# Kernel tuning notes

Measured on AMD Instinct MI355X. Metric: run time of the kernel, lower is better.

## Reference

```python
import jax, jax.numpy as jnp
import numpy as np
import math


def _unfold(x, k, s, p):
    # torch nn.Unfold: output [B, C*k*k, L] with channel-major (c, kh, kw) ordering,
    # which matches lax.conv_general_dilated_patches channel ordering.
    patches = jax.lax.conv_general_dilated_patches(
        x, (k, k), (s, s), [(p, p), (p, p)],
        dimension_numbers=('NCHW', 'OIHW', 'NCHW'))
    B, C, H, W = patches.shape
    return patches.reshape(B, C, H * W).transpose(0, 2, 1)  # [B, L, C*k*k]


def _ln(x, g, b):
    mu = x.mean(-1, keepdims=True)
    var = ((x - mu) ** 2).mean(-1, keepdims=True)
    return (x - mu) * jax.lax.rsqrt(var + 1e-5) * g + b


def _prm_exp(x, w):
    # FAVOR+ positive random-feature map: exp(w@x - |x|^2/2)/sqrt(m)
    m = w.shape[0]
    xd = (x * x).sum(-1, keepdims=True) * 0.5          # [B,T,1]
    wtx = jnp.einsum('btd,md->btm', x, w)              # [B,T,m]
    return jnp.exp(wtx - xd) / jnp.sqrt(jnp.float32(m))


def _performer(x, p):
    (kqv_w, kqv_b, proj_w, proj_b, ln1_g, ln1_b, ln2_g, ln2_b,
     m1_w, m1_b, m2_w, m2_b, rf_w) = p
    emb = proj_w.shape[0]
    xn = _ln(x, ln1_g, ln1_b)
    kqv = xn @ kqv_w + kqv_b
    k, q, v = kqv[..., :emb], kqv[..., emb:2 * emb], kqv[..., 2 * emb:]
    kp, qp = _prm_exp(k, rf_w), _prm_exp(q, rf_w)      # [B,T,m]
    D = jnp.einsum('btm,bm->bt', qp, kp.sum(1))[..., None]   # [B,T,1]
    kptv = jnp.einsum('btn,btm->bnm', v, kp)                 # [B,emb,m]
    y = jnp.einsum('btm,bnm->btn', qp, kptv) / (D + 1e-8)    # [B,T,emb]
    y = v + (y @ proj_w + proj_b)                            # dropout = identity (eval)
    h = jax.nn.gelu(_ln(y, ln2_g, ln2_b) @ m1_w + m1_b, approximate=False) @ m2_w + m2_b
    return y + h


def setup_inputs() -> dict:
    key = jax.random.key(0)
    B, emb, m = 64, 64, 32

    def lin(k, din, dout):
        return jax.random.normal(k, (din, dout), jnp.float32) / np.sqrt(din).astype(np.float32)

    def orth(seed, dim_in):
        a = np.random.default_rng(seed).standard_normal((dim_in, m))
        q, _ = np.linalg.qr(a)  # columns orthonormal
        return jnp.asarray((q[:, :m].T * np.sqrt(m)).astype(np.float32))  # [m, emb]

    inp = {"x": jax.random.normal(jax.random.fold_in(key, 0), (B, 3, 224, 224), jnp.float32)}
    for i, d in ((1, 147), (2, 576)):
        pre = f"p{i}_"
        k1, k2, k3, k4 = jax.random.split(jax.random.fold_in(key, i), 4)
        inp[pre + "kqv_w"] = lin(k1, d, 3 * emb); inp[pre + "kqv_b"] = jnp.zeros(3 * emb, jnp.float32)
        inp[pre + "proj_w"] = lin(k2, emb, emb);  inp[pre + "proj_b"] = jnp.zeros(emb, jnp.float32)
        inp[pre + "ln1_g"] = jnp.ones(d, jnp.float32);   inp[pre + "ln1_b"] = jnp.zeros(d, jnp.float32)
        inp[pre + "ln2_g"] = jnp.ones(emb, jnp.float32); inp[pre + "ln2_b"] = jnp.zeros(emb, jnp.float32)
        inp[pre + "m1_w"] = lin(k3, emb, emb); inp[pre + "m1_b"] = jnp.zeros(emb, jnp.float32)
        inp[pre + "m2_w"] = lin(k4, emb, emb); inp[pre + "m2_b"] = jnp.zeros(emb, jnp.float32)
        inp[pre + "rf"] = orth(100 + i, emb)
    inp["proj_w"] = lin(jax.random.fold_in(key, 99), 576, 768)
    inp["proj_b"] = jnp.zeros(768, jnp.float32)
    return inp


def reference(x,
              p1_kqv_w, p1_kqv_b, p1_proj_w, p1_proj_b, p1_ln1_g, p1_ln1_b,
              p1_ln2_g, p1_ln2_b, p1_m1_w, p1_m1_b, p1_m2_w, p1_m2_b, p1_rf,
              p2_kqv_w, p2_kqv_b, p2_proj_w, p2_proj_b, p2_ln1_g, p2_ln1_b,
              p2_ln2_g, p2_ln2_b, p2_m1_w, p2_m1_b, p2_m2_w, p2_m2_b, p2_rf,
              proj_w, proj_b):
    p1 = (p1_kqv_w, p1_kqv_b, p1_proj_w, p1_proj_b, p1_ln1_g, p1_ln1_b,
          p1_ln2_g, p1_ln2_b, p1_m1_w, p1_m1_b, p1_m2_w, p1_m2_b, p1_rf)
    p2 = (p2_kqv_w, p2_kqv_b, p2_proj_w, p2_proj_b, p2_ln1_g, p2_ln1_b,
          p2_ln2_g, p2_ln2_b, p2_m1_w, p2_m1_b, p2_m2_w, p2_m2_b, p2_rf)
    h = _unfold(x, 7, 4, 2)                 # [B, 3136, 147]
    h = _performer(h, p1)                   # [B, 3136, 64]
    B, T, C = h.shape
    s = int(math.isqrt(T))
    h = h.transpose(0, 2, 1).reshape(B, C, s, s)   # [B,64,56,56]
    h = _unfold(h, 3, 2, 1)                 # [B, 784, 576]
    h = _performer(h, p2)                   # [B, 784, 64]
    B, T, C = h.shape
    s = int(math.isqrt(T))
    h = h.transpose(0, 2, 1).reshape(B, C, s, s)   # [B,64,28,28]
    h = _unfold(h, 3, 2, 1)                 # [B, 196, 576]
    return h @ proj_w + proj_b              # [B, 196, 768]
```

## Files before the change

kernel.cpp:

```cpp
#include <hip/hip_runtime.h>
#include <hip/hip_bf16.h>

#define NB 64
#define T1 3136
#define T2 784
#define T3 196
#define D1 147
#define D2 576

#define KP1 160
#define KS1 168
#define KS2 584
#define KQ2 72

typedef __attribute__((ext_vector_type(8))) short bf16x8;
typedef __attribute__((ext_vector_type(4))) float f32x4;

__device__ __forceinline__ unsigned short f2bf(float v) {
    unsigned int u = __float_as_uint(v);
    return (unsigned short)((u + 0x7FFFu + ((u >> 16) & 1u)) >> 16);
}

__device__ __forceinline__ float waveReduceSum(float v) {
#pragma unroll
    for (int off = 32; off > 0; off >>= 1) v += __shfl_down(v, off, 64);
    return __shfl(v, 0, 64);
}

__global__ __launch_bounds__(192) void prep_sums(
    const float* __restrict__ w, const float* __restrict__ g,
    const float* __restrict__ bb, const float* __restrict__ kqvb,
    float* __restrict__ s2, float* __restrict__ s3, int D)
{
    const int col = threadIdx.x;
    const int d0 = blockIdx.x * 16;
    const int d1 = (d0 + 16 < D) ? d0 + 16 : D;
    float a2 = 0.f, a3 = 0.f;
    for (int d = d0; d < d1; ++d) {
        const float wv = w[d * 192 + col];
        a2 += wv * g[d];
        a3 += wv * bb[d];
    }
    if (blockIdx.x == 0) a3 += kqvb[col];
    atomicAdd(&s2[col], a2);
    atomicAdd(&s3[col], a3);
}

__global__ __launch_bounds__(256) void prep_wt(
    const float* __restrict__ w, const float* __restrict__ g,
    unsigned short* __restrict__ hi, unsigned short* __restrict__ lo,
    int D, int K, int N)
{
    const int i = blockIdx.x * 256 + threadIdx.x;
    if (i >= N * K) return;
    const int n = i / K, k = i % K;
    const float v = (k < D) ? w[k * N + n] * (g ? g[k] : 1.f) : 0.f;
    const unsigned short h = f2bf(v);
    const float hf = __uint_as_float((unsigned int)h << 16);
    const size_t pidx = (size_t)((n >> 4) * (K >> 5) + (k >> 5)) * 512
                      + (size_t)((((k >> 3) & 3) * 16 + (n & 15)) * 8 + (k & 7));
    hi[pidx] = h;
    lo[pidx] = f2bf(v - hf);
}

__global__ __launch_bounds__(256) void prep_rf(
    const float* __restrict__ rf,
    unsigned short* __restrict__ hi, unsigned short* __restrict__ lo)
{
    const int i = blockIdx.x * 256 + threadIdx.x;
    if (i >= 2048) return;
    const int n = i >> 6, k = i & 63;
    const float v = rf[i];
    const unsigned short h = f2bf(v);
    const float hf = __uint_as_float((unsigned int)h << 16);
    const int pidx = ((n >> 4) * 2 + (k >> 5)) * 512
                   + ((((k >> 3) & 3) * 16 + (n & 15)) * 8 + (k & 7));
    hi[pidx] = h;
    lo[pidx] = f2bf(v - hf);
}

__global__ __launch_bounds__(256) void front1(
    const float* __restrict__ x,
    const unsigned short* __restrict__ wt_hi,
    const unsigned short* __restrict__ wt_lo,
    const float* __restrict__ s2v, const float* __restrict__ s3v,
    const unsigned short* __restrict__ rf_hi,
    const unsigned short* __restrict__ rf_lo,
    float* __restrict__ kp, float* __restrict__ qp,
    float* __restrict__ v_out)
{
    const int tok0 = blockIdx.x * 32;
    const int b = tok0 / T1;
    const int tbase = tok0 % T1;
    const int tid = threadIdx.x;
    const int wv = tid >> 6, l = tid & 63;
    const int l15 = l & 15, lg = l >> 4;

    __shared__ __align__(16) unsigned short Abuf[2 * 32 * KS1];
    __shared__ float ps_sum[256], ps_sq[256];
    __shared__ float mu_s[32], rs_s[32], xd_s[64];

    unsigned short* A_hi = Abuf;
    unsigned short* A_lo = Abuf + 32 * KS1;
    unsigned short* kqh = Abuf;
    unsigned short* kql = Abuf + 64 * KQ2;

    { const int m = tid >> 3, j = tid & 7;
      const int t = tbase + m;
      const int py = t / 56, px = t % 56;
      const int iy0 = py * 4 - 2, ix0 = px * 4 - 2;
      float sm = 0.f, sq = 0.f;
      for (int d = j; d < KS1; d += 8) {
          float val = 0.f;
          if (d < D1) {
              const int cc = d / 49, r = d % 49, ki = r / 7, kj = r % 7;
              const int iy = iy0 + ki, ix = ix0 + kj;
              if (iy >= 0 && iy < 224 && ix >= 0 && ix < 224)
                  val = x[((b * 3 + cc) * 224 + iy) * 224 + ix];
          }
          sm += val; sq += val * val;
          const unsigned short h = f2bf(val);
          A_hi[m * KS1 + d] = h;
          A_lo[m * KS1 + d] = f2bf(val - __uint_as_float((unsigned int)h << 16));
      }
      ps_sum[tid] = sm; ps_sq[tid] = sq; }
    __syncthreads();
    if (tid < 32) {
        float s = 0.f, s2 = 0.f;
#pragma unroll
        for (int j2 = 0; j2 < 8; ++j2) { s += ps_sum[tid*8+j2]; s2 += ps_sq[tid*8+j2]; }
        const float mu = s * (1.f / D1);
        mu_s[tid] = mu; rs_s[tid] = rsqrtf(s2 * (1.f / D1) - mu * mu + 1e-5f);
    }

    f32x4 acc[2][3];
    { const f32x4 z = {0.f, 0.f, 0.f, 0.f};
#pragma unroll
      for (int mt = 0; mt < 2; ++mt)
#pragma unroll
        for (int nt = 0; nt < 3; ++nt) acc[mt][nt] = z; }

    for (int ks = 0; ks < 5; ++ks) {
        const int ko = ks * 32 + 8 * lg;
        const bf16x8 ah0 = *(const bf16x8*)&A_hi[l15 * KS1 + ko];
        const bf16x8 ah1 = *(const bf16x8*)&A_hi[(16 + l15) * KS1 + ko];
        const bf16x8 al0 = *(const bf16x8*)&A_lo[l15 * KS1 + ko];
        const bf16x8 al1 = *(const bf16x8*)&A_lo[(16 + l15) * KS1 + ko];
#pragma unroll
        for (int nt = 0; nt < 3; ++nt) {
            const size_t wo = ((size_t)((3 * wv + nt) * 5 + ks) << 9) + (size_t)(l << 3);
            const bf16x8 bh = *(const bf16x8*)&wt_hi[wo];
            const bf16x8 bl = *(const bf16x8*)&wt_lo[wo];
            acc[0][nt] = __builtin_amdgcn_mfma_f32_16x16x32_bf16(ah0, bh, acc[0][nt], 0, 0, 0);
            acc[1][nt] = __builtin_amdgcn_mfma_f32_16x16x32_bf16(ah1, bh, acc[1][nt], 0, 0, 0);
            acc[0][nt] = __builtin_amdgcn_mfma_f32_16x16x32_bf16(al0, bh, acc[0][nt], 0, 0, 0);
            acc[1][nt] = __builtin_amdgcn_mfma_f32_16x16x32_bf16(al1, bh, acc[1][nt], 0, 0, 0);
            acc[0][nt] = __builtin_amdgcn_mfma_f32_16x16x32_bf16(ah0, bl, acc[0][nt], 0, 0, 0);
            acc[1][nt] = __builtin_amdgcn_mfma_f32_16x16x32_bf16(ah1, bl, acc[1][nt], 0, 0, 0);
        }
    }
    __syncthreads();

    float xk[2][4], xq[2][4];
#pragma unroll
    for (int mt = 0; mt < 2; ++mt)
#pragma unroll
        for (int r = 0; r < 4; ++r) { xk[mt][r] = 0.f; xq[mt][r] = 0.f; }

#pragma unroll
    for (int nt = 0; nt < 3; ++nt) {
        const int col = 48 * wv + 16 * nt + l15;
        const int third = col >> 6, cc = col & 63;
        const float s2c = s2v[col], s3c = s3v[col];
#pragma unroll
        for (int mt = 0; mt < 2; ++mt) {
#pragma unroll
            for (int r = 0; r < 4; ++r) {
                const int token = mt * 16 + 4 * lg + r;
                const float o = rs_s[token] * (acc[mt][nt][r] - mu_s[token] * s2c) + s3c;
                if (third == 2) {
                    v_out[(size_t)(tok0 + token) * 64 + cc] = o;
                } else {
                    const int row = third * 32 + token;
                    const unsigned short h = f2bf(o);
                    kqh[row * KQ2 + cc] = h;
                    kql[row * KQ2 + cc] = f2bf(o - __uint_as_float((unsigned int)h << 16));
                    if (third == 0) xk[mt][r] += o * o; else xq[mt][r] += o * o;
                }
            }
        }
    }
#pragma unroll
    for (int mt = 0; mt < 2; ++mt) {
#pragma unroll
        for (int r = 0; r < 4; ++r) {
            float a = xk[mt][r], q2 = xq[mt][r];
#pragma unroll
            for (int off = 1; off < 16; off <<= 1) {
                a  += __shfl_xor(a,  off, 64);
                q2 += __shfl_xor(q2, off, 64);
            }
            if (l15 == 0) {
                const int token = mt * 16 + 4 * lg + r;
                ps_sum[wv * 64 + token]      = a;
                ps_sum[wv * 64 + 32 + token] = q2;
            }
        }
    }
    __syncthreads();
    if (tid < 64)
        xd_s[tid] = 0.5f * (ps_sum[tid] + ps_sum[64+tid] + ps_sum[128+tid] + ps_sum[192+tid]);
    __syncthreads();

    f32x4 pacc[2];
    { const f32x4 z = {0.f, 0.f, 0.f, 0.f}; pacc[0] = z; pacc[1] = z; }
#pragma unroll
    for (int ks = 0; ks < 2; ++ks) {
        const int ko = ks * 32 + 8 * lg;
        const bf16x8 ah = *(const bf16x8*)&kqh[(16 * wv + l15) * KQ2 + ko];
        const bf16x8 al = *(const bf16x8*)&kql[(16 * wv + l15) * KQ2 + ko];
#pragma unroll
        for (int nt = 0; nt < 2; ++nt) {
            const int wo = (nt * 2 + ks) * 512 + l * 8;
            const bf16x8 bh = *(const bf16x8*)&rf_hi[wo];
            const bf16x8 bl = *(const bf16x8*)&rf_lo[wo];
            pacc[nt] = __builtin_amdgcn_mfma_f32_16x16x32_bf16(ah, bh, pacc[nt], 0, 0, 0);
            pacc[nt] = __builtin_amdgcn_mfma_f32_16x16x32_bf16(al, bh, pacc[nt], 0, 0, 0);
            pacc[nt] = __builtin_amdgcn_mfma_f32_16x16x32_bf16(ah, bl, pacc[nt], 0, 0, 0);
        }
    }
#pragma unroll
    for (int nt = 0; nt < 2; ++nt) {
#pragma unroll
        for (int r = 0; r < 4; ++r) {
            const int row = 16 * wv + 4 * lg + r;
            const int half = row >> 5, token = row & 31;
            const float p = expf(pacc[nt][r] - xd_s[row]) * 0.1767766952966369f;
            (half ? qp : kp)[(size_t)(tok0 + token) * 32 + nt * 16 + l15] = p;
        }
    }
}

__global__ __launch_bounds__(256) void front2(
    const float* __restrict__ src,
    const unsigned short* __restrict__ wt_hi,
    const unsigned short* __restrict__ wt_lo,
    const float* __restrict__ s2v, const float* __restrict__ s3v,
    const unsigned short* __restrict__ rf_hi,
    const unsigned short* __restrict__ rf_lo,
    float* __restrict__ kp, float* __restrict__ qp,
    float* __restrict__ v_out)
{
    const int tok0 = blockIdx.x * 16;
    const int b = tok0 / T2;
    const int tbase = tok0 % T2;
    const int tid = threadIdx.x;
    const int wv = tid >> 6, l = tid & 63;
    const int l15 = l & 15, lg = l >> 4;

    __shared__ __align__(16) unsigned short Abuf[2 * 16 * KS2];
    __shared__ float ps_sum[256], ps_sq[256];
    __shared__ float mu_s[16], rs_s[16], xd_s[32];

    unsigned short* A_hi = Abuf;
    unsigned short* A_lo = Abuf + 16 * KS2;
    unsigned short* kqh = Abuf;
    unsigned short* kql = Abuf + 32 * KQ2;

    { const int g16 = tid >> 4, ch = tid & 15;
      const int tmine = tbase + g16;
      const int py = tmine / 28, px = tmine % 28;
      const int iy0 = py * 2 - 1, ix0 = px * 2 - 1;
      const float* srcb = src + (size_t)b * T1 * 64 + ch;
      unsigned short* Ah = &A_hi[g16 * KS2];
      unsigned short* Al = &A_lo[g16 * KS2];
      float sm = 0.f, sq = 0.f;
#pragma unroll
      for (int r = 0; r < 9; ++r) {
          const int iy = iy0 + r / 3, ix = ix0 + r % 3;
          const bool ok = (iy >= 0 && iy < 56 && ix >= 0 && ix < 56);
          const float* sp = srcb + (size_t)(iy * 56 + ix) * 64;
#pragma unroll
          for (int c = 0; c < 4; ++c) {
              const float val = ok ? sp[c * 16] : 0.f;
              sm += val; sq += val * val;
              const int d = (c * 16 + ch) * 9 + r;
              const unsigned short h = f2bf(val);
              Ah[d] = h;
              Al[d] = f2bf(val - __uint_as_float((unsigned int)h << 16));
          }
      }
      ps_sum[tid] = sm; ps_sq[tid] = sq; }
    __syncthreads();
    if (tid < 16) {
        float s = 0.f, s2 = 0.f;
#pragma unroll
        for (int j = 0; j < 16; ++j) { s += ps_sum[tid*16+j]; s2 += ps_sq[tid*16+j]; }
        const float mu = s * (1.f / D2);
        mu_s[tid] = mu; rs_s[tid] = rsqrtf(s2 * (1.f / D2) - mu * mu + 1e-5f);
    }

    f32x4 acc[3];
    { const f32x4 z = {0.f, 0.f, 0.f, 0.f};
#pragma unroll
      for (int nt = 0; nt < 3; ++nt) acc[nt] = z; }

    for (int ks = 0; ks < 18; ++ks) {
        const int ko = ks * 32 + 8 * lg;
        const bf16x8 ah = *(const bf16x8*)&A_hi[l15 * KS2 + ko];
        const bf16x8 al = *(const bf16x8*)&A_lo[l15 * KS2 + ko];
#pragma unroll
        for (int nt = 0; nt < 3; ++nt) {
            const size_t wo = ((size_t)((3 * wv + nt) * 18 + ks) << 9) + (size_t)(l << 3);
            const bf16x8 bh = *(const bf16x8*)&wt_hi[wo];
            const bf16x8 bl = *(const bf16x8*)&wt_lo[wo];
            acc[nt] = __builtin_amdgcn_mfma_f32_16x16x32_bf16(ah, bh, acc[nt], 0, 0, 0);
            acc[nt] = __builtin_amdgcn_mfma_f32_16x16x32_bf16(al, bh, acc[nt], 0, 0, 0);
            acc[nt] = __builtin_amdgcn_mfma_f32_16x16x32_bf16(ah, bl, acc[nt], 0, 0, 0);
        }
    }
    __syncthreads();

    float xk[4], xq[4];
#pragma unroll
    for (int r = 0; r < 4; ++r) { xk[r] = 0.f; xq[r] = 0.f; }

#pragma unroll
    for (int nt = 0; nt < 3; ++nt) {
        const int col = 48 * wv + 16 * nt + l15;
        const int third = col >> 6, cc = col & 63;
        const float s2c = s2v[col], s3c = s3v[col];
#pragma unroll
        for (int r = 0; r < 4; ++r) {
            const int token = 4 * lg + r;
            const float o = rs_s[token] * (acc[nt][r] - mu_s[token] * s2c) + s3c;
            if (third == 2) {
                v_out[(size_t)(tok0 + token) * 64 + cc] = o;
            } else {
                const int row = third * 16 + token;
                const unsigned short h = f2bf(o);
                kqh[row * KQ2 + cc] = h;
                kql[row * KQ2 + cc] = f2bf(o - __uint_as_float((unsigned int)h << 16));
                if (third == 0) xk[r] += o * o; else xq[r] += o * o;
            }
        }
    }
#pragma unroll
    for (int r = 0; r < 4; ++r) {
        float a = xk[r], q2 = xq[r];
#pragma unroll
        for (int off = 1; off < 16; off <<= 1) {
            a  += __shfl_xor(a,  off, 64);
            q2 += __shfl_xor(q2, off, 64);
        }
        if (l15 == 0) {
            const int token = 4 * lg + r;
            ps_sum[wv * 64 + token]      = a;
            ps_sum[wv * 64 + 16 + token] = q2;
        }
    }
    __syncthreads();
    if (tid < 32)
        xd_s[tid] = 0.5f * (ps_sum[tid] + ps_sum[64+tid] + ps_sum[128+tid] + ps_sum[192+tid]);
    __syncthreads();

    const int mt = wv >> 1, ntp = wv & 1;
    f32x4 pacc;
    { const f32x4 z = {0.f, 0.f, 0.f, 0.f}; pacc = z; }
#pragma unroll
    for (int ks = 0; ks < 2; ++ks) {
        const int ko = ks * 32 + 8 * lg;
        const bf16x8 ah = *(const bf16x8*)&kqh[(16 * mt + l15) * KQ2 + ko];
        const bf16x8 al = *(const bf16x8*)&kql[(16 * mt + l15) * KQ2 + ko];
        const int wo = (ntp * 2 + ks) * 512 + l * 8;
        const bf16x8 bh = *(const bf16x8*)&rf_hi[wo];
        const bf16x8 bl = *(const bf16x8*)&rf_lo[wo];
        pacc = __builtin_amdgcn_mfma_f32_16x16x32_bf16(ah, bh, pacc, 0, 0, 0);
        pacc = __builtin_amdgcn_mfma_f32_16x16x32_bf16(al, bh, pacc, 0, 0, 0);
        pacc = __builtin_amdgcn_mfma_f32_16x16x32_bf16(ah, bl, pacc, 0, 0, 0);
    }
#pragma unroll
    for (int r = 0; r < 4; ++r) {
        const int row = 16 * mt + 4 * lg + r;
        const int half = row >> 4, token = row & 15;
        const float p = expf(pacc[r] - xd_s[row]) * 0.1767766952966369f;
        (half ? qp : kp)[(size_t)(tok0 + token) * 32 + ntp * 16 + l15] = p;
    }
}

template <int T, int S>
__global__ __launch_bounds__(256) void reduce_kv(
    const float* __restrict__ kp, const float* __restrict__ v,
    float* __restrict__ ksum, float* __restrict__ kptv)
{
    const int b = blockIdx.x / S, s = blockIdx.x % S;
    const int chunk = T / S;
    const int tid = threadIdx.x;
    __shared__ float kp_s[8][32];
    __shared__ float v_s[8][64];
    float acc[8] = {0.f, 0.f, 0.f, 0.f, 0.f, 0.f, 0.f, 0.f};
    float ks = 0.f;
    const int n = tid >> 2;
    const int mb = (tid & 3) * 8;
    const float* kpb = kp + (size_t)b * T * 32;
    const float* vb  = v  + (size_t)b * T * 64;

    for (int t0 = s * chunk; t0 < (s + 1) * chunk; t0 += 8) {
        kp_s[tid >> 5][tid & 31] = kpb[(t0 + (tid >> 5)) * 32 + (tid & 31)];
        {
            const int i0 = tid * 2, i1 = tid * 2 + 1;
            v_s[i0 >> 6][i0 & 63] = vb[(t0 + (i0 >> 6)) * 64 + (i0 & 63)];
            v_s[i1 >> 6][i1 & 63] = vb[(t0 + (i1 >> 6)) * 64 + (i1 & 63)];
        }
        __syncthreads();
#pragma unroll
        for (int tt = 0; tt < 8; ++tt) {
            const float vv = v_s[tt][n];
#pragma unroll
            for (int i = 0; i < 8; ++i) acc[i] += vv * kp_s[tt][mb + i];
        }
        if (tid < 32) {
#pragma unroll
            for (int tt = 0; tt < 8; ++tt) ks += kp_s[tt][tid];
        }
        __syncthreads();
    }
#pragma unroll
    for (int i = 0; i < 8; ++i) atomicAdd(&kptv[(b * 64 + n) * 32 + mb + i], acc[i]);
    if (tid < 32) atomicAdd(&ksum[b * 32 + tid], ks);
}

template <int T>
__global__ __launch_bounds__(128) void epilogue(
    const float* __restrict__ qp, const float* __restrict__ v,
    const float* __restrict__ ksum, const float* __restrict__ kptv,
    const unsigned short* __restrict__ pw_hi, const unsigned short* __restrict__ pw_lo,
    const float* __restrict__ proj_b,
    const float* __restrict__ ln2_g, const float* __restrict__ ln2_b,
    const unsigned short* __restrict__ m1_hi, const unsigned short* __restrict__ m1_lo,
    const float* __restrict__ m1_b,
    const unsigned short* __restrict__ m2_hi, const unsigned short* __restrict__ m2_lo,
    const float* __restrict__ m2_b,
    float* __restrict__ out)
{
    const int sub = threadIdx.x >> 6;
    const int l = threadIdx.x & 63;
    const int l15 = l & 15, lg = l >> 4;
    const int tok0 = blockIdx.x * 32 + sub * 16;
    const int b = tok0 / T;

    __shared__ __align__(16) float qp_s[2][16 * 36];
    __shared__ __align__(16) unsigned short Ah[2][16 * KQ2];
    __shared__ __align__(16) unsigned short Al[2][16 * KQ2];
    __shared__ float ks_s[2][32];
    __shared__ float D_s[2][16];

    for (int idx = l; idx < 512; idx += 64)
        qp_s[sub][(idx >> 5) * 36 + (idx & 31)] = qp[(size_t)tok0 * 32 + idx];
    if (l < 32) ks_s[sub][l] = ksum[b * 32 + l];
    __syncthreads();
    if (l < 16) {
        float D = 1e-8f;
        for (int r = 0; r < 32; ++r) D += qp_s[sub][l * 36 + r] * ks_s[sub][r];
        D_s[sub][l] = D;
    }
    float4 kv4[8];
#pragma unroll
    for (int g = 0; g < 8; ++g)
        kv4[g] = *(const float4*)&kptv[(size_t)(b * 64 + l) * 32 + 4 * g];
    __syncthreads();

    unsigned short* ah = Ah[sub];
    unsigned short* al = Al[sub];
#pragma unroll
    for (int m = 0; m < 16; ++m) {
        const float4* q4 = (const float4*)&qp_s[sub][m * 36];
        float a = 0.f;
#pragma unroll
        for (int g = 0; g < 8; ++g) {
            const float4 qv = q4[g];
            a += qv.x*kv4[g].x + qv.y*kv4[g].y + qv.z*kv4[g].z + qv.w*kv4[g].w;
        }
        a /= D_s[sub][m];
        const unsigned short h = f2bf(a);
        ah[m * KQ2 + l] = h;
        al[m * KQ2 + l] = f2bf(a - __uint_as_float((unsigned int)h << 16));
    }
    __syncthreads();

    f32x4 y[4];
    { const f32x4 z = {0.f, 0.f, 0.f, 0.f};
#pragma unroll
      for (int nt = 0; nt < 4; ++nt) y[nt] = z; }
#pragma unroll
    for (int ks = 0; ks < 2; ++ks) {
        const int ko = ks * 32 + 8 * lg;
        const bf16x8 fa = *(const bf16x8*)&ah[l15 * KQ2 + ko];
        const bf16x8 fl = *(const bf16x8*)&al[l15 * KQ2 + ko];
#pragma unroll
        for (int nt = 0; nt < 4; ++nt) {
            const int wo = (nt * 2 + ks) * 512 + l * 8;
            const bf16x8 bh = *(const bf16x8*)&pw_hi[wo];
            const bf16x8 bl = *(const bf16x8*)&pw_lo[wo];
            y[nt] = __builtin_amdgcn_mfma_f32_16x16x32_bf16(fa, bh, y[nt], 0, 0, 0);
            y[nt] = __builtin_amdgcn_mfma_f32_16x16x32_bf16(fl, bh, y[nt], 0, 0, 0);
            y[nt] = __builtin_amdgcn_mfma_f32_16x16x32_bf16(fa, bl, y[nt], 0, 0, 0);
        }
    }
#pragma unroll
    for (int nt = 0; nt < 4; ++nt) {
        const int col = 16 * nt + l15;
        const float pb = proj_b[col];
#pragma unroll
        for (int r = 0; r < 4; ++r)
            y[nt][r] += pb + v[(size_t)(tok0 + 4 * lg + r) * 64 + col];
    }
    __syncthreads();

    { float g2c[4], b2c[4];
#pragma unroll
      for (int nt = 0; nt < 4; ++nt) { g2c[nt] = ln2_g[16*nt+l15]; b2c[nt] = ln2_b[16*nt+l15]; }
#pragma unroll
      for (int r = 0; r < 4; ++r) {
          float s = y[0][r] + y[1][r] + y[2][r] + y[3][r];
          float s2 = y[0][r]*y[0][r] + y[1][r]*y[1][r] + y[2][r]*y[2][r] + y[3][r]*y[3][r];
#pragma unroll
          for (int off = 1; off < 16; off <<= 1) {
              s  += __shfl_xor(s,  off, 64);
              s2 += __shfl_xor(s2, off, 64);
          }
          const float mu = s * (1.f / 64.f);
          const float rs = rsqrtf(s2 * (1.f / 64.f) - mu * mu + 1e-5f);
          const int row = (4 * lg + r) * KQ2;
#pragma unroll
          for (int nt = 0; nt < 4; ++nt) {
              const float z = (y[nt][r] - mu) * rs * g2c[nt] + b2c[nt];
              const unsigned short h = f2bf(z);
              ah[row + 16 * nt + l15] = h;
              al[row + 16 * nt + l15] = f2bf(z - __uint_as_float((unsigned int)h << 16));
          }
      } }
    __syncthreads();

    f32x4 hf[4];
    { const f32x4 z = {0.f, 0.f, 0.f, 0.f};
#pragma unroll
      for (int nt = 0; nt < 4; ++nt) hf[nt] = z; }
#pragma unroll
    for (int ks = 0; ks < 2; ++ks) {
        const int ko = ks * 32 + 8 * lg;
        const bf16x8 fa = *(const bf16x8*)&ah[l15 * KQ2 + ko];
        const bf16x8 fl = *(const bf16x8*)&al[l15 * KQ2 + ko];
#pragma unroll
        for (int nt = 0; nt < 4; ++nt) {
            const int wo = (nt * 2 + ks) * 512 + l * 8;
            const bf16x8 bh = *(const bf16x8*)&m1_hi[wo];
            const bf16x8 bl = *(const bf16x8*)&m1_lo[wo];
            hf[nt] = __builtin_amdgcn_mfma_f32_16x16x32_bf16(fa, bh, hf[nt], 0, 0, 0);
            hf[nt] = __builtin_amdgcn_mfma_f32_16x16x32_bf16(fl, bh, hf[nt], 0, 0, 0);
            hf[nt] = __builtin_amdgcn_mfma_f32_16x16x32_bf16(fa, bl, hf[nt], 0, 0, 0);
        }
    }
    __syncthreads();
#pragma unroll
    for (int nt = 0; nt < 4; ++nt) {
        const float b1 = m1_b[16 * nt + l15];
#pragma unroll
        for (int r = 0; r < 4; ++r) {
            const float t = hf[nt][r] + b1;
            const float gl = 0.5f * t * (1.f + erff(t * 0.7071067811865476f));
            const unsigned short h = f2bf(gl);
            const int idx = (4 * lg + r) * KQ2 + 16 * nt + l15;
            ah[idx] = h;
            al[idx] = f2bf(gl - __uint_as_float((unsigned int)h << 16));
        }
    }
    __syncthreads();

    f32x4 oacc[4];
    { const f32x4 z = {0.f, 0.f, 0.f, 0.f};
#pragma unroll
      for (int nt = 0; nt < 4; ++nt) oacc[nt] = z; }
#pragma unroll
    for (int ks = 0; ks < 2; ++ks) {
        const int ko = ks * 32 + 8 * lg;
        const bf16x8 fa = *(const bf16x8*)&ah[l15 * KQ2 + ko];
        const bf16x8 fl = *(const bf16x8*)&al[l15 * KQ2 + ko];
#pragma unroll
        for (int nt = 0; nt < 4; ++nt) {
            const int wo = (nt * 2 + ks) * 512 + l * 8;
            const bf16x8 bh = *(const bf16x8*)&m2_hi[wo];
            const bf16x8 bl = *(const bf16x8*)&m2_lo[wo];
            oacc[nt] = __builtin_amdgcn_mfma_f32_16x16x32_bf16(fa, bh, oacc[nt], 0, 0, 0);
            oacc[nt] = __builtin_amdgcn_mfma_f32_16x16x32_bf16(fl, bh, oacc[nt], 0, 0, 0);
            oacc[nt] = __builtin_amdgcn_mfma_f32_16x16x32_bf16(fa, bl, oacc[nt], 0, 0, 0);
        }
    }
#pragma unroll
    for (int nt = 0; nt < 4; ++nt) {
        const int col = 16 * nt + l15;
        const float b2v = m2_b[col];
#pragma unroll
        for (int r = 0; r < 4; ++r)
            out[(size_t)(tok0 + 4 * lg + r) * 64 + col] = y[nt][r] + oacc[nt][r] + b2v;
    }
}

__global__ __launch_bounds__(256) void final_proj(
    const float* __restrict__ o2,
    const unsigned short* __restrict__ wt_hi,
    const unsigned short* __restrict__ wt_lo,
    const float* __restrict__ bias,
    float* __restrict__ out)
{
    const int tok0 = blockIdx.x * 16;
    const int tid = threadIdx.x;
    const int wv = tid >> 6, l = tid & 63;
    const int l15 = l & 15, lg = l >> 4;

    __shared__ __align__(16) unsigned short Abuf[2 * 16 * KS2];
    unsigned short* A_hi = Abuf;
    unsigned short* A_lo = Abuf + 16 * KS2;

    { const int cl = tid & 15, grp = tid >> 4;
      for (int k = 0; k < 4; ++k) {
#pragma unroll
        for (int ii = 0; ii < 9; ++ii) {
            const int u = grp + ii * 16;
            const int m = u / 9, r = u % 9;
            const int tok = tok0 + m, bb = tok / T3, tt = tok % T3;
            const int py = tt / 14, px = tt % 14;
            const int iy = py * 2 - 1 + r / 3, ix = px * 2 - 1 + r % 3;
            float val = 0.f;
            if (iy >= 0 && iy < 28 && ix >= 0 && ix < 28)
                val = o2[(size_t)(bb * T2 + iy * 28 + ix) * 64 + k * 16 + cl];
            const int d = k * 144 + cl * 9 + r;
            const unsigned short h = f2bf(val);
            A_hi[m * KS2 + d] = h;
            A_lo[m * KS2 + d] = f2bf(val - __uint_as_float((unsigned int)h << 16));
        }
      }
    }
    __syncthreads();

    f32x4 acc[12];
    { const f32x4 z = {0.f, 0.f, 0.f, 0.f};
#pragma unroll
      for (int nt = 0; nt < 12; ++nt) acc[nt] = z; }

    for (int ks = 0; ks < 18; ++ks) {
        const int ko = ks * 32 + 8 * lg;
        const bf16x8 ah = *(const bf16x8*)&A_hi[l15 * KS2 + ko];
        const bf16x8 al = *(const bf16x8*)&A_lo[l15 * KS2 + ko];
#pragma unroll
        for (int nt = 0; nt < 12; ++nt) {
            const size_t wo = ((size_t)((12 * wv + nt) * 18 + ks) << 9) + (size_t)(l << 3);
            const bf16x8 bh = *(const bf16x8*)&wt_hi[wo];
            const bf16x8 bl = *(const bf16x8*)&wt_lo[wo];
            acc[nt] = __builtin_amdgcn_mfma_f32_16x16x32_bf16(ah, bh, acc[nt], 0, 0, 0);
            acc[nt] = __builtin_amdgcn_mfma_f32_16x16x32_bf16(al, bh, acc[nt], 0, 0, 0);
            acc[nt] = __builtin_amdgcn_mfma_f32_16x16x32_bf16(ah, bl, acc[nt], 0, 0, 0);
        }
    }

#pragma unroll
    for (int nt = 0; nt < 12; ++nt) {
        const int col = 192 * wv + 16 * nt + l15;
        const float bv = bias[col];
#pragma unroll
        for (int r = 0; r < 4; ++r) {
            const int token = 4 * lg + r;
            out[(size_t)(tok0 + token) * 768 + col] = acc[nt][r] + bv;
        }
    }
}

extern "C" void kernel_launch(void* const* d_in, const int* in_sizes, int n_in,
                              void* d_out, int out_size, void* d_ws, size_t ws_size,
                              hipStream_t stream) {
    const float* x         = (const float*)d_in[0];
    const float* p1_kqv_w  = (const float*)d_in[1];
    const float* p1_kqv_b  = (const float*)d_in[2];
    const float* p1_proj_w = (const float*)d_in[3];
    const float* p1_proj_b = (const float*)d_in[4];
    const float* p1_ln1_g  = (const float*)d_in[5];
    const float* p1_ln1_b  = (const float*)d_in[6];
    const float* p1_ln2_g  = (const float*)d_in[7];
    const float* p1_ln2_b  = (const float*)d_in[8];
    const float* p1_m1_w   = (const float*)d_in[9];
    const float* p1_m1_b   = (const float*)d_in[10];
    const float* p1_m2_w   = (const float*)d_in[11];
    const float* p1_m2_b   = (const float*)d_in[12];
    const float* p1_rf     = (const float*)d_in[13];
    const float* p2_kqv_w  = (const float*)d_in[14];
    const float* p2_kqv_b  = (const float*)d_in[15];
    const float* p2_proj_w = (const float*)d_in[16];
    const float* p2_proj_b = (const float*)d_in[17];
    const float* p2_ln1_g  = (const float*)d_in[18];
    const float* p2_ln1_b  = (const float*)d_in[19];
    const float* p2_ln2_g  = (const float*)d_in[20];
    const float* p2_ln2_b  = (const float*)d_in[21];
    const float* p2_m1_w   = (const float*)d_in[22];
    const float* p2_m1_b   = (const float*)d_in[23];
    const float* p2_m2_w   = (const float*)d_in[24];
    const float* p2_m2_b   = (const float*)d_in[25];
    const float* p2_rf     = (const float*)d_in[26];
    const float* proj_w    = (const float*)d_in[27];
    const float* proj_b    = (const float*)d_in[28];

    float* ws = (float*)d_ws;
    size_t off = 0;
    float* ksum1 = ws + off; off += (size_t)NB * 32;
    float* kptv1 = ws + off; off += (size_t)NB * 64 * 32;
    float* ksum2 = ws + off; off += (size_t)NB * 32;
    float* kptv2 = ws + off; off += (size_t)NB * 64 * 32;
    float* s2v = ws + off; off += 192;
    float* s3v = ws + off; off += 192;
    float* s2v1 = ws + off; off += 192;
    float* s3v1 = ws + off; off += 192;
    const size_t zero_bytes = off * sizeof(float);
    float* kp1 = ws + off; off += (size_t)NB * T1 * 32;
    float* qp1 = ws + off; off += (size_t)NB * T1 * 32;
    float* v1  = ws + off; off += (size_t)NB * T1 * 64;
    float* o1  = ws + off; off += (size_t)NB * T1 * 64;
    unsigned short* wt1h = (unsigned short*)(ws + off); off += (size_t)192 * KP1 / 2;
    unsigned short* wt1l = (unsigned short*)(ws + off); off += (size_t)192 * KP1 / 2;
    unsigned short* wt2h = (unsigned short*)(ws + off); off += (size_t)192 * 576 / 2;
    unsigned short* wt2l = (unsigned short*)(ws + off); off += (size_t)192 * 576 / 2;
    unsigned short* wtfh = (unsigned short*)(ws + off); off += (size_t)768 * 576 / 2;
    unsigned short* wtfl = (unsigned short*)(ws + off); off += (size_t)768 * 576 / 2;
    unsigned short* rf1h = (unsigned short*)(ws + off); off += 1024;
    unsigned short* rf1l = (unsigned short*)(ws + off); off += 1024;
    unsigned short* rf2h = (unsigned short*)(ws + off); off += 1024;
    unsigned short* rf2l = (unsigned short*)(ws + off); off += 1024;
    unsigned short* ep1[6]; unsigned short* ep2[6];
    for (int i = 0; i < 6; ++i) { ep1[i] = (unsigned short*)(ws + off); off += 2048; }
    for (int i = 0; i < 6; ++i) { ep2[i] = (unsigned short*)(ws + off); off += 2048; }
    size_t off2 = 0;
    float* kp2 = kp1 + off2; off2 += (size_t)NB * T2 * 32;
    float* qp2 = kp1 + off2; off2 += (size_t)NB * T2 * 32;
    float* v2  = kp1 + off2; off2 += (size_t)NB * T2 * 64;
    float* o2  = kp1 + off2; off2 += (size_t)NB * T2 * 64;

    hipMemsetAsync(ws, 0, zero_bytes, stream);

    prep_sums<<<(D2 + 15) / 16, 192, 0, stream>>>(p2_kqv_w, p2_ln1_g, p2_ln1_b, p2_kqv_b, s2v, s3v, D2);
    prep_sums<<<(D1 + 15) / 16, 192, 0, stream>>>(p1_kqv_w, p1_ln1_g, p1_ln1_b, p1_kqv_b, s2v1, s3v1, D1);
    prep_wt<<<(192 * KP1 + 255) / 256, 256, 0, stream>>>(p1_kqv_w, p1_ln1_g, wt1h, wt1l, D1, KP1, 192);
    prep_wt<<<(192 * 576 + 255) / 256, 256, 0, stream>>>(p2_kqv_w, p2_ln1_g, wt2h, wt2l, D2, 576, 192);
    prep_wt<<<(768 * 576 + 255) / 256, 256, 0, stream>>>(proj_w, nullptr, wtfh, wtfl, D2, 576, 768);
    prep_rf<<<8, 256, 0, stream>>>(p1_rf, rf1h, rf1l);
    prep_rf<<<8, 256, 0, stream>>>(p2_rf, rf2h, rf2l);
    prep_wt<<<16, 256, 0, stream>>>(p1_proj_w, nullptr, ep1[0], ep1[1], 64, 64, 64);
    prep_wt<<<16, 256, 0, stream>>>(p1_m1_w,   nullptr, ep1[2], ep1[3], 64, 64, 64);
    prep_wt<<<16, 256, 0, stream>>>(p1_m2_w,   nullptr, ep1[4], ep1[5], 64, 64, 64);
    prep_wt<<<16, 256, 0, stream>>>(p2_proj_w, nullptr, ep2[0], ep2[1], 64, 64, 64);
    prep_wt<<<16, 256, 0, stream>>>(p2_m1_w,   nullptr, ep2[2], ep2[3], 64, 64, 64);
    prep_wt<<<16, 256, 0, stream>>>(p2_m2_w,   nullptr, ep2[4], ep2[5], 64, 64, 64);

    front1<<<NB * T1 / 32, 256, 0, stream>>>(x, wt1h, wt1l, s2v1, s3v1, rf1h, rf1l, kp1, qp1, v1);
    reduce_kv<T1, 14><<<NB * 14, 256, 0, stream>>>(kp1, v1, ksum1, kptv1);
    epilogue<T1><<<NB * T1 / 32, 128, 0, stream>>>(qp1, v1, ksum1, kptv1,
                                                   ep1[0], ep1[1], p1_proj_b, p1_ln2_g, p1_ln2_b,
                                                   ep1[2], ep1[3], p1_m1_b, ep1[4], ep1[5], p1_m2_b, o1);
    front2<<<NB * T2 / 16, 256, 0, stream>>>(o1, wt2h, wt2l, s2v, s3v, rf2h, rf2l, kp2, qp2, v2);
    reduce_kv<T2, 7><<<NB * 7, 256, 0, stream>>>(kp2, v2, ksum2, kptv2);
    epilogue<T2><<<NB * T2 / 32, 128, 0, stream>>>(qp2, v2, ksum2, kptv2,
                                                   ep2[0], ep2[1], p2_proj_b, p2_ln2_g, p2_ln2_b,
                                                   ep2[2], ep2[3], p2_m1_b, ep2[4], ep2[5], p2_m2_b, o2);
    final_proj<<<NB * T3 / 16, 256, 0, stream>>>(o2, wtfh, wtfl, proj_b, (float*)d_out);
}
```

Before: 684.5 us.

## Fuse k-feature/value reduction into front kernels with per-block atomics

Each front kernel now keeps its k random-feature tile in shared memory and immediately reduces it against the block's v values into kptv and ksum via atomics. This drops the separate reduce_kv kernels and the global round trip for kp. In exchange it issues far more global atomic adds, contended across many blocks on the same per-batch accumulators.

```diff
diff --git a/kernel.cpp b/kernel.cpp
--- a/kernel.cpp
+++ b/kernel.cpp
@@ -86,8 +86,9 @@
     const float* __restrict__ s2v, const float* __restrict__ s3v,
     const unsigned short* __restrict__ rf_hi,
     const unsigned short* __restrict__ rf_lo,
-    float* __restrict__ kp, float* __restrict__ qp,
-    float* __restrict__ v_out)
+    float* __restrict__ qp,
+    float* __restrict__ v_out,
+    float* __restrict__ ksum, float* __restrict__ kptv)
 {
     const int tok0 = blockIdx.x * 32;
     const int b = tok0 / T1;
@@ -229,16 +230,39 @@
             pacc[nt] = __builtin_amdgcn_mfma_f32_16x16x32_bf16(ah, bl, pacc[nt], 0, 0, 0);
         }
     }
+    __syncthreads();
+
+    float* kps = (float*)Abuf;
 #pragma unroll
     for (int nt = 0; nt < 2; ++nt) {
 #pragma unroll
         for (int r = 0; r < 4; ++r) {
             const int row = 16 * wv + 4 * lg + r;
-            const int half = row >> 5, token = row & 31;
             const float p = expf(pacc[nt][r] - xd_s[row]) * 0.1767766952966369f;
-            (half ? qp : kp)[(size_t)(tok0 + token) * 32 + nt * 16 + l15] = p;
-        }
-    }
+            if (row < 32)
+                kps[row * 36 + nt * 16 + l15] = p;
+            else
+                qp[(size_t)(tok0 + (row & 31)) * 32 + nt * 16 + l15] = p;
+        }
+    }
+    __syncthreads();
+
+    { const int n = tid >> 2, mb = (tid & 3) * 8;
+      const float* vb = v_out + (size_t)tok0 * 64;
+      float racc[8] = {0.f,0.f,0.f,0.f,0.f,0.f,0.f,0.f};
+      for (int t = 0; t < 32; ++t) {
+          const float vv = vb[t * 64 + n];
+#pragma unroll
+          for (int i = 0; i < 8; ++i) racc[i] += vv * kps[t * 36 + mb + i];
+      }
+      float* kb = &kptv[((size_t)b * 64 + n) * 32 + mb];
+#pragma unroll
+      for (int i = 0; i < 8; ++i) atomicAdd(&kb[i], racc[i]);
+      if (tid < 32) {
+          float ks2 = 0.f;
+          for (int t = 0; t < 32; ++t) ks2 += kps[t * 36 + tid];
+          atomicAdd(&ksum[b * 32 + tid], ks2);
+      } }
 }
 
 __global__ __launch_bounds__(256) void front2(
@@ -248,8 +272,9 @@
     const float* __restrict__ s2v, const float* __restrict__ s3v,
     const unsigned short* __restrict__ rf_hi,
     const unsigned short* __restrict__ rf_lo,
-    float* __restrict__ kp, float* __restrict__ qp,
-    float* __restrict__ v_out)
+    float* __restrict__ qp,
+    float* __restrict__ v_out,
+    float* __restrict__ ksum, float* __restrict__ kptv)
 {
     const int tok0 = blockIdx.x * 16;
     const int b = tok0 / T2;
@@ -379,55 +404,36 @@
         pacc = __builtin_amdgcn_mfma_f32_16x16x32_bf16(al, bh, pacc, 0, 0, 0);
         pacc = __builtin_amdgcn_mfma_f32_16x16x32_bf16(ah, bl, pacc, 0, 0, 0);
     }
+    __syncthreads();
+
+    float* kps = (float*)Abuf;
 #pragma unroll
     for (int r = 0; r < 4; ++r) {
         const int row = 16 * mt + 4 * lg + r;
-        const int half = row >> 4, token = row & 15;
         const float p = expf(pacc[r] - xd_s[row]) * 0.1767766952966369f;
-        (half ? qp : kp)[(size_t)(tok0 + token) * 32 + ntp * 16 + l15] = p;
-    }
-}
-
-template <int T, int S>
-__global__ __launch_bounds__(256) void reduce_kv(
-    const float* __restrict__ kp, const float* __restrict__ v,
-    float* __restrict__ ksum, float* __restrict__ kptv)
-{
-    const int b = blockIdx.x / S, s = blockIdx.x % S;
-    const int chunk = T / S;
-    const int tid = threadIdx.x;
-    __shared__ float kp_s[8][32];
-    __shared__ float v_s[8][64];
-    float acc[8] = {0.f, 0.f, 0.f, 0.f, 0.f, 0.f, 0.f, 0.f};
-    float ks = 0.f;
-    const int n = tid >> 2;
-    const int mb = (tid & 3) * 8;
-    const float* kpb = kp + (size_t)b * T * 32;
-    const float* vb  = v  + (size_t)b * T * 64;
-
-    for (int t0 = s * chunk; t0 < (s + 1) * chunk; t0 += 8) {
-        kp_s[tid >> 5][tid & 31] = kpb[(t0 + (tid >> 5)) * 32 + (tid & 31)];
-        {
-            const int i0 = tid * 2, i1 = tid * 2 + 1;
-            v_s[i0 >> 6][i0 & 63] = vb[(t0 + (i0 >> 6)) * 64 + (i0 & 63)];
-            v_s[i1 >> 6][i1 & 63] = vb[(t0 + (i1 >> 6)) * 64 + (i1 & 63)];
-        }
-        __syncthreads();
-#pragma unroll
-        for (int tt = 0; tt < 8; ++tt) {
-            const float vv = v_s[tt][n];
-#pragma unroll
-            for (int i = 0; i < 8; ++i) acc[i] += vv * kp_s[tt][mb + i];
-        }
-        if (tid < 32) {
-#pragma unroll
-            for (int tt = 0; tt < 8; ++tt) ks += kp_s[tt][tid];
-        }
-        __syncthreads();
-    }
-#pragma unroll
-    for (int i = 0; i < 8; ++i) atomicAdd(&kptv[(b * 64 + n) * 32 + mb + i], acc[i]);
-    if (tid < 32) atomicAdd(&ksum[b * 32 + tid], ks);
+        if (row < 16)
+            kps[row * 36 + ntp * 16 + l15] = p;
+        else
+            qp[(size_t)(tok0 + (row & 15)) * 32 + ntp * 16 + l15] = p;
+    }
+    __syncthreads();
+
+    { const int n = tid >> 2, mb = (tid & 3) * 8;
+      const float* vb = v_out + (size_t)tok0 * 64;
+      float racc[8] = {0.f,0.f,0.f,0.f,0.f,0.f,0.f,0.f};
+      for (int t = 0; t < 16; ++t) {
+          const float vv = vb[t * 64 + n];
+#pragma unroll
+          for (int i = 0; i < 8; ++i) racc[i] += vv * kps[t * 36 + mb + i];
+      }
+      float* kb = &kptv[((size_t)b * 64 + n) * 32 + mb];
+#pragma unroll
+      for (int i = 0; i < 8; ++i) atomicAdd(&kb[i], racc[i]);
+      if (tid < 32) {
+          float ks2 = 0.f;
+          for (int t = 0; t < 16; ++t) ks2 += kps[t * 36 + tid];
+          atomicAdd(&ksum[b * 32 + tid], ks2);
+      } }
 }
 
 template <int T>
@@ -741,6 +747,7 @@
     float* qp2 = kp1 + off2; off2 += (size_t)NB * T2 * 32;
     float* v2  = kp1 + off2; off2 += (size_t)NB * T2 * 64;
     float* o2  = kp1 + off2; off2 += (size_t)NB * T2 * 64;
+    (void)kp1; (void)kp2;
 
     hipMemsetAsync(ws, 0, zero_bytes, stream);
 
@@ -758,13 +765,13 @@
     prep_wt<<<16, 256, 0, stream>>>(p2_m1_w,   nullptr, ep2[2], ep2[3], 64, 64, 64);
     prep_wt<<<16, 256, 0, stream>>>(p2_m2_w,   nullptr, ep2[4], ep2[5], 64, 64, 64);
 
-    front1<<<NB * T1 / 32, 256, 0, stream>>>(x, wt1h, wt1l, s2v1, s3v1, rf1h, rf1l, kp1, qp1, v1);
-    reduce_kv<T1, 14><<<NB * 14, 256, 0, stream>>>(kp1, v1, ksum1, kptv1);
+    front1<<<NB * T1 / 32, 256, 0, stream>>>(x, wt1h, wt1l, s2v1, s3v1, rf1h, rf1l,
+                                             qp1, v1, ksum1, kptv1);
     epilogue<T1><<<NB * T1 / 32, 128, 0, stream>>>(qp1, v1, ksum1, kptv1,
                                                    ep1[0], ep1[1], p1_proj_b, p1_ln2_g, p1_ln2_b,
                                                    ep1[2], ep1[3], p1_m1_b, ep1[4], ep1[5], p1_m2_b, o1);
-    front2<<<NB * T2 / 16, 256, 0, stream>>>(o1, wt2h, wt2l, s2v, s3v, rf2h, rf2l, kp2, qp2, v2);
-    reduce_kv<T2, 7><<<NB * 7, 256, 0, stream>>>(kp2, v2, ksum2, kptv2);
+    front2<<<NB * T2 / 16, 256, 0, stream>>>(o1, wt2h, wt2l, s2v, s3v, rf2h, rf2l,
+                                             qp2, v2, ksum2, kptv2);
     epilogue<T2><<<NB * T2 / 32, 128, 0, stream>>>(qp2, v2, ksum2, kptv2,
                                                    ep2[0], ep2[1], p2_proj_b, p2_ln2_g, p2_ln2_b,
                                                    ep2[2], ep2[3], p2_m1_b, ep2[4], ep2[5], p2_m2_b, o2);
```

Measured after the change: 997.4 us. 1.46x slower.
